# Performance work log

Hardware: AMD Instinct MI355X
Metric: run time of the kernel (lower is better)

Reference implementation:

```python
import jax, jax.numpy as jnp
import numpy as np
from jax import lax

B, T, S = 64, 512, 500
M, E, P, H, A = 80, 512, 256, 1024, 128
F_LOC, K_LOC = 32, 31
P_ATT_DROP, P_DEC_DROP, P_PRENET_DROP = 0.1, 0.1, 0.5
NEG_INF = -1e9


def _dropout(x, p, key):
    keep = jax.random.bernoulli(key, 1.0 - p, x.shape)
    return jnp.where(keep, x / (1.0 - p), jnp.zeros_like(x))


def _lstm_cell(x, h, c, w_ih, w_hh, b_ih, b_hh):
    # torch LSTMCell gate order: i, f, g, o
    gates = x @ w_ih.T + b_ih + h @ w_hh.T + b_hh
    i, f, g, o = jnp.split(gates, 4, axis=-1)
    c_new = jax.nn.sigmoid(f) * c + jax.nn.sigmoid(i) * jnp.tanh(g)
    h_new = jax.nn.sigmoid(o) * jnp.tanh(c_new)
    return h_new, c_new


def setup_inputs() -> dict:
    key = jax.random.key(0)
    ks = jax.random.split(key, 20)
    s = 0.02
    return dict(
        memory=jax.random.normal(ks[0], (B, T, E), jnp.float32),
        memory_lengths=jax.random.randint(ks[1], (B,), T // 2, T + 1),
        decoder_inputs=jax.random.normal(ks[2], (B, S, M), jnp.float32),
        prenet_w1=jax.random.normal(ks[3], (P, M), jnp.float32) * s,
        prenet_w2=jax.random.normal(ks[4], (P, P), jnp.float32) * s,
        attn_rnn_w_ih=jax.random.normal(ks[5], (4 * H, P + E), jnp.float32) * s,
        attn_rnn_w_hh=jax.random.normal(ks[6], (4 * H, H), jnp.float32) * s,
        attn_rnn_b_ih=jnp.zeros((4 * H,), jnp.float32),
        attn_rnn_b_hh=jnp.zeros((4 * H,), jnp.float32),
        dec_rnn_w_ih=jax.random.normal(ks[7], (4 * H, H + E), jnp.float32) * s,
        dec_rnn_w_hh=jax.random.normal(ks[8], (4 * H, H), jnp.float32) * s,
        dec_rnn_b_ih=jnp.zeros((4 * H,), jnp.float32),
        dec_rnn_b_hh=jnp.zeros((4 * H,), jnp.float32),
        attn_query_w=jax.random.normal(ks[9], (A, H), jnp.float32) * s,
        attn_memory_w=jax.random.normal(ks[10], (A, E), jnp.float32) * s,
        attn_v=jax.random.normal(ks[11], (A,), jnp.float32) * s,
        loc_conv_w=jax.random.normal(ks[12], (F_LOC, 2, K_LOC), jnp.float32) * s,
        loc_dense_w=jax.random.normal(ks[13], (A, F_LOC), jnp.float32) * s,
        proj_w=jax.random.normal(ks[14], (M, H + E), jnp.float32) * s,
        proj_b=jnp.zeros((M,), jnp.float32),
        gate_w=jax.random.normal(ks[15], (1, H + E), jnp.float32) * s,
        gate_b=jnp.zeros((1,), jnp.float32),
    )


def _forward(memory, memory_lengths, decoder_inputs,
             prenet_w1, prenet_w2,
             attn_rnn_w_ih, attn_rnn_w_hh, attn_rnn_b_ih, attn_rnn_b_hh,
             dec_rnn_w_ih, dec_rnn_w_hh, dec_rnn_b_ih, dec_rnn_b_hh,
             attn_query_w, attn_memory_w, attn_v, loc_conv_w, loc_dense_w,
             proj_w, proj_b, gate_w, gate_b):
    dt = memory.dtype
    # processed memory: [B, T, A]
    processed_memory = jnp.einsum('bte,ae->bta', memory, attn_memory_w)
    # mask True at padded positions
    pad_mask = jnp.arange(T)[None, :] >= memory_lengths[:, None]  # [B, T]

    # prenet over [S+1, B, M] (go frame + teacher-forced inputs); always-on dropout 0.5
    go = jnp.zeros((1, B, M), dt)
    x = jnp.concatenate([go, jnp.transpose(decoder_inputs, (1, 0, 2))], axis=0)
    x = _dropout(jax.nn.relu(x @ prenet_w1.T), P_PRENET_DROP, jax.random.key(101))
    x = _dropout(jax.nn.relu(x @ prenet_w2.T), P_PRENET_DROP, jax.random.key(102))
    prenet_out = x[:S]  # [S, B, P]

    drop_base = jax.random.key(7)
    pad = (K_LOC - 1) // 2

    def step(carry, xs):
        ah, ac, dh, dc, aw, awc, ctx = carry
        xt, t_idx = xs
        # attention RNN
        cell_in = jnp.concatenate([xt, ctx], axis=-1)  # [B, P+E]
        ah, ac = _lstm_cell(cell_in, ah, ac, attn_rnn_w_ih, attn_rnn_w_hh,
                            attn_rnn_b_ih, attn_rnn_b_hh)
        ah = _dropout(ah, P_ATT_DROP, jax.random.fold_in(drop_base, 2 * t_idx))
        # location-sensitive attention
        aw_cat = jnp.stack([aw, awc], axis=1)  # [B, 2, T]
        loc = lax.conv_general_dilated(aw_cat, loc_conv_w, (1,), [(pad, pad)],
                                       dimension_numbers=('NCH', 'OIH', 'NCH'))  # [B, F, T]
        processed_loc = jnp.einsum('bft,af->bta', loc, loc_dense_w)  # [B, T, A]
        q = (ah @ attn_query_w.T)[:, None, :]  # [B, 1, A]
        energies = jnp.tanh(q + processed_loc + processed_memory) @ attn_v  # [B, T]
        energies = jnp.where(pad_mask, NEG_INF, energies)
        aw = jax.nn.softmax(energies, axis=-1)
        ctx = jnp.einsum('bt,bte->be', aw, memory)
        awc = awc + aw
        # decoder RNN
        dec_in = jnp.concatenate([ah, ctx], axis=-1)  # [B, H+E]
        dh, dc = _lstm_cell(dec_in, dh, dc, dec_rnn_w_ih, dec_rnn_w_hh,
                            dec_rnn_b_ih, dec_rnn_b_hh)
        dh = _dropout(dh, P_DEC_DROP, jax.random.fold_in(drop_base, 2 * t_idx + 1))
        hc = jnp.concatenate([dh, ctx], axis=-1)  # [B, H+E]
        mel = hc @ proj_w.T + proj_b  # [B, M]
        gate = (hc @ gate_w.T + gate_b)[:, 0]  # [B]
        return (ah, ac, dh, dc, aw, awc, ctx), (mel, gate, aw)

    z = lambda *shape: jnp.zeros(shape, dt)
    carry0 = (z(B, H), z(B, H), z(B, H), z(B, H), z(B, T), z(B, T), z(B, E))
    _, (mels, gates, aligns) = lax.scan(step, carry0, (prenet_out, jnp.arange(S)))
    mel_outputs = jnp.transpose(mels, (1, 0, 2))      # [B, S, M]
    gate_outputs = jnp.transpose(gates, (1, 0))       # [B, S]
    alignments = jnp.transpose(aligns, (1, 0, 2))     # [B, S, T]
    return mel_outputs, gate_outputs, alignments


def reference(memory, memory_lengths, decoder_inputs,
              prenet_w1, prenet_w2,
              attn_rnn_w_ih, attn_rnn_w_hh, attn_rnn_b_ih, attn_rnn_b_hh,
              dec_rnn_w_ih, dec_rnn_w_hh, dec_rnn_b_ih, dec_rnn_b_hh,
              attn_query_w, attn_memory_w, attn_v, loc_conv_w, loc_dense_w,
              proj_w, proj_b, gate_w, gate_b):
    return _forward(memory, memory_lengths, decoder_inputs,
                    prenet_w1, prenet_w2,
                    attn_rnn_w_ih, attn_rnn_w_hh, attn_rnn_b_ih, attn_rnn_b_hh,
                    dec_rnn_w_ih, dec_rnn_w_hh, dec_rnn_b_ih, dec_rnn_b_hh,
                    attn_query_w, attn_memory_w, attn_v, loc_conv_w, loc_dense_w,
                    proj_w, proj_b, gate_w, gate_b)
```

## Files before the change

### kernel.cpp

```cpp
#include <hip/hip_runtime.h>
#include <cstdint>


__device__ __forceinline__ void tf2x32(uint32_t k0, uint32_t k1, uint32_t& x0, uint32_t& x1) {
  uint32_t ks2 = k0 ^ k1 ^ 0x1BD11BDAu;
  x0 += k0; x1 += k1;
#define TFR(r) { x0 += x1; x1 = (x1 << (r)) | (x1 >> (32 - (r))); x1 ^= x0; }
  TFR(13) TFR(15) TFR(26) TFR(6)
  x0 += k1; x1 += ks2 + 1u;
  TFR(17) TFR(29) TFR(16) TFR(24)
  x0 += ks2; x1 += k0 + 2u;
  TFR(13) TFR(15) TFR(26) TFR(6)
  x0 += k0; x1 += k1 + 3u;
  TFR(17) TFR(29) TFR(16) TFR(24)
  x0 += k1; x1 += ks2 + 4u;
  TFR(13) TFR(15) TFR(26) TFR(6)
  x0 += ks2; x1 += k0 + 5u;
#undef TFR
}

__device__ __forceinline__ uint32_t rng_bits(uint32_t k0, uint32_t k1, uint32_t idx) {
  uint32_t x0 = 0u, x1 = idx;
  tf2x32(k0, k1, x0, x1);
  return x0 ^ x1;
// ... 111 lines not shown
  const int jrow = jbase + row;

  float4 rx0, rx1, rw0, rw1;
  auto loadt = [&](int kb, float4& x0r, float4& x1r, float4& w0r, float4& w1r) {
    const float* xp; int xst, xof;
    if (kb < L0)            { xp = s0; xst = L0;   xof = kb; }
    else if (kb < L0 + L1)  { xp = s1; xst = L1;   xof = kb - L0; }
    else                    { xp = sh; xst = 1024; xof = kb - L0 - L1; }
    const float* xr = xp + (size_t)row * xst + xof + q8;
    x0r = *(const float4*)xr; x1r = *(const float4*)(xr + 4);
    const float* wp; int wst, wof;
    if (kb < LIH) { wp = wih; wst = LIH;  wof = kb; }
    else          { wp = whh; wst = 1024; wof = kb - LIH; }
    const float* wr = wp + (size_t)jrow * wst + wof + q8;
    w0r = *(const float4*)wr; w1r = *(const float4*)(wr + 4);
  };

  loadt(k0, rx0, rx1, rw0, rw1);
  float acc[4][4] = {};
  for (int c = 0; c < NC; ++c) {
    __syncthreads();
#pragma unroll
    for (int i = 0; i < 4; i++) {
      xs[q8 + i][row]     = ((const float*)&rx0)[i];
      xs[q8 + 4 + i][row] = ((const float*)&rx1)[i];
      ws[q8 + i][row]     = ((const float*)&rw0)[i];
      ws[q8 + 4 + i][row] = ((const float*)&rw1)[i];
    }
    __syncthreads();
    if (c + 1 < NC) loadt(k0 + (c + 1) * 32, rx0, rx1, rw0, rw1);
#pragma unroll
    for (int kk = 0; kk < 32; kk++) {
      float4 xv = *(const float4*)&xs[kk][bq * 4];
      float4 wv = *(const float4*)&ws[kk][jq * 4];
      acc[0][0] = fmaf(wv.x, xv.x, acc[0][0]); acc[0][1] = fmaf(wv.x, xv.y, acc[0][1]);
      acc[0][2] = fmaf(wv.x, xv.z, acc[0][2]); acc[0][3] = fmaf(wv.x, xv.w, acc[0][3]);
      acc[1][0] = fmaf(wv.y, xv.x, acc[1][0]); acc[1][1] = fmaf(wv.y, xv.y, acc[1][1]);
      acc[1][2] = fmaf(wv.y, xv.z, acc[1][2]); acc[1][3] = fmaf(wv.y, xv.w, acc[1][3]);
      acc[2][0] = fmaf(wv.z, xv.x, acc[2][0]); acc[2][1] = fmaf(wv.z, xv.y, acc[2][1]);
      acc[2][2] = fmaf(wv.z, xv.z, acc[2][2]); acc[2][3] = fmaf(wv.z, xv.w, acc[2][3]);
      acc[3][0] = fmaf(wv.w, xv.x, acc[3][0]); acc[3][1] = fmaf(wv.w, xv.y, acc[3][1]);
      acc[3][2] = fmaf(wv.w, xv.z, acc[3][2]); acc[3][3] = fmaf(wv.w, xv.w, acc[3][3]);
    }
  }
  float* pbase = part + (size_t)blockIdx.y * 64 * 4096;
#pragma unroll
  for (int bb = 0; bb < 4; bb++) {
    int b = bq * 4 + bb;
    float4 o = make_float4(acc[0][bb], acc[1][bb], acc[2][bb], acc[3][bb]);
    *(float4*)&pbase[(size_t)b * 4096 + jbase + jq * 4] = o;
  }
}

__global__ __launch_bounds__(1024) void k_attn_point(
    const float* __restrict__ part,
    const float* __restrict__ bih, const float* __restrict__ bhh,
    float* __restrict__ ac, float* __restrict__ ah,
    const uint32_t* __restrict__ kf, int dsel,
    const float* __restrict__ wq, float* __restrict__ q) {
  const int b = blockIdx.x, tid = threadIdx.x;
  __shared__ float ahs[1024];
  __shared__ float qred[128][9];
  const uint32_t fk0 = kf[2 * dsel], fk1 = kf[2 * dsel + 1];
  {
    const int h = tid;
    float gi = bih[h] + bhh[h];
    float gf = bih[h + 1024] + bhh[h + 1024];
    float gg = bih[h + 2048] + bhh[h + 2048];
    float go = bih[h + 3072] + bhh[h + 3072];
    for (int ks = 0; ks < 8; ks++) {
      const float* p = part + (size_t)(ks * 64 + b) * 4096;
      gi += p[h]; gf += p[h + 1024]; gg += p[h + 2048]; go += p[h + 3072];
    }
    float c = sigmf(gf) * ac[b * 1024 + h] + sigmf(gi) * tanhf(gg);
    float hn = sigmf(go) * tanhf(c);
    ac[b * 1024 + h] = c;
    float u = rng_u01(fk0, fk1, (uint32_t)(b * 1024 + h));
    hn = (u < 0.9f) ? hn / 0.9f : 0.0f;
    ah[b * 1024 + h] = hn;
    ahs[h] = hn;
  }
  __syncthreads();
  {
    const int a = tid & 127, seg = tid >> 7;
    const float* wr = wq + (size_t)a * 1024 + seg * 128;
    const float* hs = ahs + seg * 128;
    float a0 = 0, a1 = 0, a2 = 0, a3 = 0;
#pragma unroll 8
    for (int k = 0; k < 128; k += 4) {
      float4 w4 = *(const float4*)(wr + k);
      float4 h4 = *(const float4*)(hs + k);
      a0 = fmaf(h4.x, w4.x, a0); a1 = fmaf(h4.y, w4.y, a1);
      a2 = fmaf(h4.z, w4.z, a2); a3 = fmaf(h4.w, w4.w, a3);
    }
    qred[a][seg] = (a0 + a1) + (a2 + a3);
  }
  __syncthreads();
  if (tid < 128) {
    float t = 0.f;
#pragma unroll
    for (int i = 0; i < 8; i++) t += qred[tid][i];
    q[b * 128 + tid] = t;
  }
}

__global__ __launch_bounds__(256) void k_energy(
    const float* __restrict__ aw, const float* __restrict__ awc,
    const float* __restrict__ q, const float* __restrict__ pm,
    const float* __restrict__ wconv, const float* __restrict__ wld,
    const float* __restrict__ v, const int* __restrict__ mlen,
    float* __restrict__ energ) {
  const int b = blockIdx.x;
  const int t0 = blockIdx.y * 64;
  const int tid = threadIdx.x;
  const int t = tid & 63, aq = tid >> 6;
  __shared__ float sa[2][96];
  __shared__ float sq[128], sv[128];
  __shared__ float sw[1984];
  __shared__ float sld[128][32];
  __shared__ float sloc[64][33];
  __shared__ float spart[64][4];
  for (int i = tid; i < 94; i += 256) {
    int tt = t0 - 15 + i;
    bool ok = (tt >= 0 && tt < 512);
    sa[0][i] = ok ? aw[b * 512 + tt] : 0.0f;
    sa[1][i] = ok ? awc[b * 512 + tt] : 0.0f;
  }
  if (tid < 128) { sq[tid] = q[b * 128 + tid]; sv[tid] = v[tid]; }
  for (int i = tid; i < 1984; i += 256) sw[i] = wconv[i];
  for (int i = tid; i < 4096; i += 256) ((float*)sld)[i] = wld[i];
  __syncthreads();
  const int len = mlen[b];
  const int tt = t0 + t;
  const bool act = (tt < len);
  if (act) {
    for (int f = aq * 8; f < aq * 8 + 8; f++) {
      const float* w0 = sw + f * 62;
      const float* w1 = w0 + 31;
      float a = 0;
#pragma unroll
      for (int k = 0; k < 31; k++) a += sa[0][t + k] * w0[k] + sa[1][t + k] * w1[k];
      sloc[t][f] = a;
    }
  }
  __syncthreads();
  if (act) {
    const float* pmr = pm + (size_t)(b * 512 + tt) * 128;
    float acc = 0;
    for (int a = aq * 32; a < aq * 32 + 32; a++) {
      float pl = 0;
#pragma unroll
      for (int f = 0; f < 32; f++) pl += sloc[t][f] * sld[a][f];
      float x = sq[a] + pl + pmr[a];
      float ex = __expf(2.0f * x);
      acc += sv[a] * (1.0f - 2.0f / (ex + 1.0f));
    }
    spart[t][aq] = acc;
  }
  __syncthreads();
  if (tid < 64) {
    int g = t0 + tid;
    float e = (g < len) ? (spart[tid][0] + spart[tid][1]) + (spart[tid][2] + spart[tid][3]) : -1e9f;
    energ[b * 512 + g] = e;
  }
}

__global__ __launch_bounds__(1024) void k_softmax_ctx(
    const float* __restrict__ energ, const int* __restrict__ mlen,
    const float* __restrict__ memv,
    float* __restrict__ aw, float* __restrict__ awc, float* __restrict__ ctx,
    float* __restrict__ out_align, int s) {
  const int b = blockIdx.x, tid = threadIdx.x;
  __shared__ float se[512];
  __shared__ float red[8];
  __shared__ float4 cred4[8][128];
  const int len = mlen[b];
  float x = 0.f;
  if (tid < 512) {
    float e = energ[b * 512 + tid];
    float m = e;
#pragma unroll
    for (int off = 32; off; off >>= 1) m = fmaxf(m, __shfl_xor(m, off, 64));
    if ((tid & 63) == 0) red[tid >> 6] = m;
  }
  __syncthreads();
  float maxv = fmaxf(fmaxf(fmaxf(red[0], red[1]), fmaxf(red[2], red[3])),
                     fmaxf(fmaxf(red[4], red[5]), fmaxf(red[6], red[7])));
  if (tid < 512) {
    float e = energ[b * 512 + tid];
    x = (tid < len) ? __expf(e - maxv) : 0.0f;
    float sm = x;
#pragma unroll
    for (int off = 32; off; off >>= 1) sm += __shfl_xor(sm, off, 64);
    __syncthreads();
    if ((tid & 63) == 0) red[tid >> 6] = sm;
  } else {
    __syncthreads();
  }
  __syncthreads();
  const float tot = ((red[0] + red[1]) + (red[2] + red[3])) +
                    ((red[4] + red[5]) + (red[6] + red[7]));
  if (tid < 512) {
    float awv = x / tot;
    se[tid] = awv;
    aw[b * 512 + tid] = awv;
    awc[b * 512 + tid] += awv;
    out_align[(size_t)b * 256000 + (size_t)s * 512 + tid] = awv;
  }
  __syncthreads();
  {
    const int e4 = tid & 127, tq = tid >> 7;
    const float4* mb = (const float4*)(memv + (size_t)b * 262144) + e4;
    float4 c = make_float4(0.f, 0.f, 0.f, 0.f);
    for (int t2 = tq; t2 < len; t2 += 8) {
      float w = se[t2];
      float4 mv = mb[(size_t)t2 * 128];
      c.x = fmaf(w, mv.x, c.x); c.y = fmaf(w, mv.y, c.y);
      c.z = fmaf(w, mv.z, c.z); c.w = fmaf(w, mv.w, c.w);
    }
    cred4[tq][e4] = c;
  }
  __syncthreads();
  if (tid < 128) {
    float4 c = cred4[0][tid];
#pragma unroll
    for (int i = 1; i < 8; i++) {
      float4 d = cred4[i][tid];
      c.x += d.x; c.y += d.y; c.z += d.z; c.w += d.w;
    }
    *(float4*)&ctx[b * 512 + tid * 4] = c;
  }
}

__global__ __launch_bounds__(1024) void k_dec_out(
    const float* __restrict__ part,
    const float* __restrict__ bih, const float* __restrict__ bhh,
    float* __restrict__ dc, float* __restrict__ dh,
    const uint32_t* __restrict__ kf, int dsel,
    const float* __restrict__ ctx,
    const float* __restrict__ projw, const float* __restrict__ projb,
    const float* __restrict__ gatew, const float* __restrict__ gateb,
    float* __restrict__ out_mel, float* __restrict__ out_gate, int s) {
  const int b = blockIdx.x, tid = threadIdx.x;
  __shared__ float hcs[1536];
  __shared__ float ored[128][9];
  const uint32_t fk0 = kf[2 * dsel], fk1 = kf[2 * dsel + 1];
  {
    const int h = tid;
    float gi = bih[h] + bhh[h];
    float gf = bih[h + 1024] + bhh[h + 1024];
    float gg = bih[h + 2048] + bhh[h + 2048];
    float go = bih[h + 3072] + bhh[h + 3072];
    for (int ks = 0; ks < 8; ks++) {
      const float* p = part + (size_t)(ks * 64 + b) * 4096;
      gi += p[h]; gf += p[h + 1024]; gg += p[h + 2048]; go += p[h + 3072];
    }
    float c = sigmf(gf) * dc[b * 1024 + h] + sigmf(gi) * tanhf(gg);
    float hn = sigmf(go) * tanhf(c);
    dc[b * 1024 + h] = c;
    float u = rng_u01(fk0, fk1, (uint32_t)(b * 1024 + h));
    hn = (u < 0.9f) ? hn / 0.9f : 0.0f;
    dh[b * 1024 + h] = hn;
    hcs[h] = hn;
  }
  if (tid < 512) hcs[1024 + tid] = ctx[b * 512 + tid];
  __syncthreads();
  {
    const int mm = tid & 127, seg = tid >> 7;
    if (mm <= 80) {
      const float* wr = ((mm < 80) ? (projw + (size_t)mm * 1536) : gatew) + seg * 192;
      const float* hs = hcs + seg * 192;
      float a0 = 0, a1 = 0, a2 = 0, a3 = 0;
#pragma unroll 4
      for (int k = 0; k < 192; k += 4) {
        float4 w4 = *(const float4*)(wr + k);
        float4 h4 = *(const float4*)(hs + k);
        a0 = fmaf(h4.x, w4.x, a0); a1 = fmaf(h4.y, w4.y, a1);
        a2 = fmaf(h4.z, w4.z, a2); a3 = fmaf(h4.w, w4.w, a3);
      }
      ored[mm][seg] = (a0 + a1) + (a2 + a3);
    }
  }
  __syncthreads();
  if (tid <= 80) {
    float tot = 0.f;
#pragma unroll
    for (int i = 0; i < 8; i++) tot += ored[tid][i];
    if (tid < 80) out_mel[(size_t)b * 40000 + (size_t)s * 80 + tid] = tot + projb[tid];
    else          out_gate[b * 500 + s] = tot + gateb[0];
  }
}

extern "C" void kernel_launch(void* const* d_in, const int* in_sizes, int n_in,
                              void* d_out, int out_size, void* d_ws, size_t ws_size,
                              hipStream_t stream) {
  const float* memory = (const float*)d_in[0];
  const int*   mlen   = (const int*)d_in[1];
  const float* dec_in = (const float*)d_in[2];
  const float* pw1    = (const float*)d_in[3];
  const float* pw2    = (const float*)d_in[4];
  const float* awih   = (const float*)d_in[5];
  const float* awhh   = (const float*)d_in[6];
  const float* abih   = (const float*)d_in[7];
  const float* abhh   = (const float*)d_in[8];
  const float* dwih   = (const float*)d_in[9];
  const float* dwhh   = (const float*)d_in[10];
  const float* dbih   = (const float*)d_in[11];
  const float* dbhh   = (const float*)d_in[12];
  const float* wq     = (const float*)d_in[13];
  const float* wm     = (const float*)d_in[14];
  const float* av     = (const float*)d_in[15];
  const float* wconv  = (const float*)d_in[16];
  const float* wld    = (const float*)d_in[17];
  const float* projw  = (const float*)d_in[18];
  const float* projb  = (const float*)d_in[19];
  const float* gatew  = (const float*)d_in[20];
  const float* gateb  = (const float*)d_in[21];

  float* out       = (float*)d_out;
  float* out_mel   = out;
  float* out_gate  = out + 2560000;
  float* out_align = out + 2592000;

  float* ws     = (float*)d_ws;
  float* pm     = ws;
  float* prenet = pm + 4194304;
  float* part   = prenet + 8192000;
  float* st     = part + 2097152;
  float* ah  = st;
  float* ac  = ah + 65536;
  float* dh  = ac + 65536;
  float* dc  = dh + 65536;
  float* aw  = dc + 65536;
  float* awc = aw + 32768;
  float* ctx = awc + 32768;
  float* q     = ctx + 32768;
  float* energ = q + 8192;
  uint32_t* kf = (uint32_t*)(energ + 32768);

  hipMemsetAsync(st, 0, (size_t)(4 * 65536 + 3 * 32768) * sizeof(float), stream);
  k_fold<<<4, 256, 0, stream>>>(kf);
  k_pm<<<4096, 256, 0, stream>>>(memory, wm, pm);
  k_prenet1<<<4000, 256, 0, stream>>>(dec_in, pw1, prenet);
  k_prenet2<<<4000, 256, 0, stream>>>(prenet, pw2);

  for (int s = 0; s < 500; s++) {
    k_gemm_part<<<dim3(64, 8), 256, 0, stream>>>(prenet + (size_t)s * 16384, 256,
                                                 ctx, 512, ah, awih, awhh, 768, 224, part);
    k_attn_point<<<64, 1024, 0, stream>>>(part, abih, abhh, ac, ah, kf, 2 * s, wq, q);
    k_energy<<<dim3(64, 8), 256, 0, stream>>>(aw, awc, q, pm, wconv, wld, av, mlen, energ);
    k_softmax_ctx<<<64, 1024, 0, stream>>>(energ, mlen, memory, aw, awc, ctx, out_align, s);
    k_gemm_part<<<dim3(64, 8), 256, 0, stream>>>(ah, 1024, ctx, 512, dh,
                                                 dwih, dwhh, 1536, 320, part);
    k_dec_out<<<64, 1024, 0, stream>>>(part, dbih, dbhh, dc, dh, kf, 2 * s + 1, ctx,
                                       projw, projb, gatew, gateb, out_mel, out_gate, s);
  }
}
```

Baseline: 62.82 ms.

## Fuse per-step attention, energy, softmax and decoder-output kernels into one launch

```diff
diff --git a/kernel.cpp b/kernel.cpp
--- a/kernel.cpp
+++ b/kernel.cpp
@@ -187,224 +187,58 @@
   }
 }
 
-__global__ __launch_bounds__(1024) void k_attn_point(
-    const float* __restrict__ part,
-    const float* __restrict__ bih, const float* __restrict__ bhh,
-    float* __restrict__ ac, float* __restrict__ ah,
-    const uint32_t* __restrict__ kf, int dsel,
-    const float* __restrict__ wq, float* __restrict__ q) {
-  const int b = blockIdx.x, tid = threadIdx.x;
-  __shared__ float ahs[1024];
-  __shared__ float qred[128][9];
-  const uint32_t fk0 = kf[2 * dsel], fk1 = kf[2 * dsel + 1];
+
+struct FP {
+  const float* part_a; const float* part_d;
+  const float* abih; const float* abhh;
+  const float* dbih; const float* dbhh;
+  float* ac; float* ah; float* dc; float* dh;
+  const uint32_t* kf; int s;
+  const float* wq; const float* wconv; const float* wld; const float* av;
+  const float* pm; const int* mlen;
+  float* aw; float* awc;
+  const float* memory;
+  const float* ctx_prev; float* ctx_cur;
+  const float* projw; const float* projb;
+  const float* gatew; const float* gateb;
+  float* out_mel; float* out_gate; float* out_align;
+};
+
+union FU {
+  struct { float hcs[1536]; float ored[128][9]; } mg;
+  struct { float ahs[1024]; float qred[128][9]; } ap;
+  struct { float sa[2][160]; float sloc[128][33]; float spart[128][8]; } en;
+  struct { float cred[8][128][4]; } cx;
+};
+
+__device__ __forceinline__ void dec_pointwise_melgate(
+    const FP& p, FU& u, int b, int tid, int sm1) {
+  const uint32_t fk0 = p.kf[2 * (2 * sm1 + 1)], fk1 = p.kf[2 * (2 * sm1 + 1) + 1];
   {
     const int h = tid;
-    float gi = bih[h] + bhh[h];
-    float gf = bih[h + 1024] + bhh[h + 1024];
-    float gg = bih[h + 2048] + bhh[h + 2048];
-    float go = bih[h + 3072] + bhh[h + 3072];
+    float gi = p.dbih[h] + p.dbhh[h];
+    float gf = p.dbih[h + 1024] + p.dbhh[h + 1024];
+    float gg = p.dbih[h + 2048] + p.dbhh[h + 2048];
+    float go = p.dbih[h + 3072] + p.dbhh[h + 3072];
     for (int ks = 0; ks < 8; ks++) {
-      const float* p = part + (size_t)(ks * 64 + b) * 4096;
-      gi += p[h]; gf += p[h + 1024]; gg += p[h + 2048]; go += p[h + 3072];
-    }
-    float c = sigmf(gf) * ac[b * 1024 + h] + sigmf(gi) * tanhf(gg);
+      const float* pp = p.part_d + (size_t)(ks * 64 + b) * 4096;
+      gi += pp[h]; gf += pp[h + 1024]; gg += pp[h + 2048]; go += pp[h + 3072];
+    }
+    float c = sigmf(gf) * p.dc[b * 1024 + h] + sigmf(gi) * tanhf(gg);
     float hn = sigmf(go) * tanhf(c);
-    ac[b * 1024 + h] = c;
-    float u = rng_u01(fk0, fk1, (uint32_t)(b * 1024 + h));
-    hn = (u < 0.9f) ? hn / 0.9f : 0.0f;
-    ah[b * 1024 + h] = hn;
-    ahs[h] = hn;
-  }
-  __syncthreads();
-  {
-    const int a = tid & 127, seg = tid >> 7;
-    const float* wr = wq + (size_t)a * 1024 + seg * 128;
-    const float* hs = ahs + seg * 128;
-    float a0 = 0, a1 = 0, a2 = 0, a3 = 0;
-#pragma unroll 8
-    for (int k = 0; k < 128; k += 4) {
-      float4 w4 = *(const float4*)(wr + k);
-      float4 h4 = *(const float4*)(hs + k);
-      a0 = fmaf(h4.x, w4.x, a0); a1 = fmaf(h4.y, w4.y, a1);
-      a2 = fmaf(h4.z, w4.z, a2); a3 = fmaf(h4.w, w4.w, a3);
-    }
-    qred[a][seg] = (a0 + a1) + (a2 + a3);
-  }
-  __syncthreads();
-  if (tid < 128) {
-    float t = 0.f;
-#pragma unroll
-    for (int i = 0; i < 8; i++) t += qred[tid][i];
-    q[b * 128 + tid] = t;
-  }
-}
-
-__global__ __launch_bounds__(256) void k_energy(
-    const float* __restrict__ aw, const float* __restrict__ awc,
-    const float* __restrict__ q, const float* __restrict__ pm,
-    const float* __restrict__ wconv, const float* __restrict__ wld,
-    const float* __restrict__ v, const int* __restrict__ mlen,
-    float* __restrict__ energ) {
-  const int b = blockIdx.x;
-  const int t0 = blockIdx.y * 64;
-  const int tid = threadIdx.x;
-  const int t = tid & 63, aq = tid >> 6;
-  __shared__ float sa[2][96];
-  __shared__ float sq[128], sv[128];
-  __shared__ float sw[1984];
-  __shared__ float sld[128][32];
-  __shared__ float sloc[64][33];
-  __shared__ float spart[64][4];
-  for (int i = tid; i < 94; i += 256) {
-    int tt = t0 - 15 + i;
-    bool ok = (tt >= 0 && tt < 512);
-    sa[0][i] = ok ? aw[b * 512 + tt] : 0.0f;
-    sa[1][i] = ok ? awc[b * 512 + tt] : 0.0f;
-  }
-  if (tid < 128) { sq[tid] = q[b * 128 + tid]; sv[tid] = v[tid]; }
-  for (int i = tid; i < 1984; i += 256) sw[i] = wconv[i];
-  for (int i = tid; i < 4096; i += 256) ((float*)sld)[i] = wld[i];
-  __syncthreads();
-  const int len = mlen[b];
-  const int tt = t0 + t;
-  const bool act = (tt < len);
-  if (act) {
-    for (int f = aq * 8; f < aq * 8 + 8; f++) {
-      const float* w0 = sw + f * 62;
-      const float* w1 = w0 + 31;
-      float a = 0;
-#pragma unroll
-      for (int k = 0; k < 31; k++) a += sa[0][t + k] * w0[k] + sa[1][t + k] * w1[k];
-      sloc[t][f] = a;
-    }
-  }
-  __syncthreads();
-  if (act) {
-    const float* pmr = pm + (size_t)(b * 512 + tt) * 128;
-    float acc = 0;
-    for (int a = aq * 32; a < aq * 32 + 32; a++) {
-      float pl = 0;
-#pragma unroll
-      for (int f = 0; f < 32; f++) pl += sloc[t][f] * sld[a][f];
-      float x = sq[a] + pl + pmr[a];
-      float ex = __expf(2.0f * x);
-      acc += sv[a] * (1.0f - 2.0f / (ex + 1.0f));
-    }
-    spart[t][aq] = acc;
-  }
-  __syncthreads();
-  if (tid < 64) {
-    int g = t0 + tid;
-    float e = (g < len) ? (spart[tid][0] + spart[tid][1]) + (spart[tid][2] + spart[tid][3]) : -1e9f;
-    energ[b * 512 + g] = e;
-  }
-}
-
-__global__ __launch_bounds__(1024) void k_softmax_ctx(
-    const float* __restrict__ energ, const int* __restrict__ mlen,
-    const float* __restrict__ memv,
-    float* __restrict__ aw, float* __restrict__ awc, float* __restrict__ ctx,
-    float* __restrict__ out_align, int s) {
-  const int b = blockIdx.x, tid = threadIdx.x;
-  __shared__ float se[512];
-  __shared__ float red[8];
-  __shared__ float4 cred4[8][128];
-  const int len = mlen[b];
-  float x = 0.f;
-  if (tid < 512) {
-    float e = energ[b * 512 + tid];
-    float m = e;
-#pragma unroll
-    for (int off = 32; off; off >>= 1) m = fmaxf(m, __shfl_xor(m, off, 64));
-    if ((tid & 63) == 0) red[tid >> 6] = m;
-  }
-  __syncthreads();
-  float maxv = fmaxf(fmaxf(fmaxf(red[0], red[1]), fmaxf(red[2], red[3])),
-                     fmaxf(fmaxf(red[4], red[5]), fmaxf(red[6], red[7])));
-  if (tid < 512) {
-    float e = energ[b * 512 + tid];
-    x = (tid < len) ? __expf(e - maxv) : 0.0f;
-    float sm = x;
-#pragma unroll
-    for (int off = 32; off; off >>= 1) sm += __shfl_xor(sm, off, 64);
-    __syncthreads();
-    if ((tid & 63) == 0) red[tid >> 6] = sm;
-  } else {
-    __syncthreads();
-  }
-  __syncthreads();
-  const float tot = ((red[0] + red[1]) + (red[2] + red[3])) +
-                    ((red[4] + red[5]) + (red[6] + red[7]));
-  if (tid < 512) {
-    float awv = x / tot;
-    se[tid] = awv;
-    aw[b * 512 + tid] = awv;
-    awc[b * 512 + tid] += awv;
-    out_align[(size_t)b * 256000 + (size_t)s * 512 + tid] = awv;
-  }
-  __syncthreads();
-  {
-    const int e4 = tid & 127, tq = tid >> 7;
-    const float4* mb = (const float4*)(memv + (size_t)b * 262144) + e4;
-    float4 c = make_float4(0.f, 0.f, 0.f, 0.f);
-    for (int t2 = tq; t2 < len; t2 += 8) {
-      float w = se[t2];
-      float4 mv = mb[(size_t)t2 * 128];
-      c.x = fmaf(w, mv.x, c.x); c.y = fmaf(w, mv.y, c.y);
-      c.z = fmaf(w, mv.z, c.z); c.w = fmaf(w, mv.w, c.w);
-    }
-    cred4[tq][e4] = c;
-  }
-  __syncthreads();
-  if (tid < 128) {
-    float4 c = cred4[0][tid];
-#pragma unroll
-    for (int i = 1; i < 8; i++) {
-      float4 d = cred4[i][tid];
-      c.x += d.x; c.y += d.y; c.z += d.z; c.w += d.w;
-    }
-    *(float4*)&ctx[b * 512 + tid * 4] = c;
-  }
-}
-
-__global__ __launch_bounds__(1024) void k_dec_out(
-    const float* __restrict__ part,
-    const float* __restrict__ bih, const float* __restrict__ bhh,
-    float* __restrict__ dc, float* __restrict__ dh,
-    const uint32_t* __restrict__ kf, int dsel,
-    const float* __restrict__ ctx,
-    const float* __restrict__ projw, const float* __restrict__ projb,
-    const float* __restrict__ gatew, const float* __restrict__ gateb,
-    float* __restrict__ out_mel, float* __restrict__ out_gate, int s) {
-  const int b = blockIdx.x, tid = threadIdx.x;
-  __shared__ float hcs[1536];
-  __shared__ float ored[128][9];
-  const uint32_t fk0 = kf[2 * dsel], fk1 = kf[2 * dsel + 1];
-  {
-    const int h = tid;
-    float gi = bih[h] + bhh[h];
-    float gf = bih[h + 1024] + bhh[h + 1024];
-    float gg = bih[h + 2048] + bhh[h + 2048];
-    float go = bih[h + 3072] + bhh[h + 3072];
-    for (int ks = 0; ks < 8; ks++) {
-      const float* p = part + (size_t)(ks * 64 + b) * 4096;
-      gi += p[h]; gf += p[h + 1024]; gg += p[h + 2048]; go += p[h + 3072];
-    }
-    float c = sigmf(gf) * dc[b * 1024 + h] + sigmf(gi) * tanhf(gg);
-    float hn = sigmf(go) * tanhf(c);
-    dc[b * 1024 + h] = c;
-    float u = rng_u01(fk0, fk1, (uint32_t)(b * 1024 + h));
-    hn = (u < 0.9f) ? hn / 0.9f : 0.0f;
-    dh[b * 1024 + h] = hn;
-    hcs[h] = hn;
-  }
-  if (tid < 512) hcs[1024 + tid] = ctx[b * 512 + tid];
+    p.dc[b * 1024 + h] = c;
+    float uu = rng_u01(fk0, fk1, (uint32_t)(b * 1024 + h));
+    hn = (uu < 0.9f) ? hn / 0.9f : 0.0f;
+    p.dh[b * 1024 + h] = hn;
+    u.mg.hcs[h] = hn;
+  }
+  if (tid < 512) u.mg.hcs[1024 + tid] = p.ctx_prev[b * 512 + tid];
   __syncthreads();
   {
     const int mm = tid & 127, seg = tid >> 7;
     if (mm <= 80) {
-      const float* wr = ((mm < 80) ? (projw + (size_t)mm * 1536) : gatew) + seg * 192;
-      const float* hs = hcs + seg * 192;
+      const float* wr = ((mm < 80) ? (p.projw + (size_t)mm * 1536) : p.gatew) + seg * 192;
+      const float* hs = u.mg.hcs + seg * 192;
       float a0 = 0, a1 = 0, a2 = 0, a3 = 0;
 #pragma unroll 4
       for (int k = 0; k < 192; k += 4) {
@@ -413,17 +247,196 @@
         a0 = fmaf(h4.x, w4.x, a0); a1 = fmaf(h4.y, w4.y, a1);
         a2 = fmaf(h4.z, w4.z, a2); a3 = fmaf(h4.w, w4.w, a3);
       }
-      ored[mm][seg] = (a0 + a1) + (a2 + a3);
+      u.mg.ored[mm][seg] = (a0 + a1) + (a2 + a3);
     }
   }
   __syncthreads();
   if (tid <= 80) {
     float tot = 0.f;
 #pragma unroll
-    for (int i = 0; i < 8; i++) tot += ored[tid][i];
-    if (tid < 80) out_mel[(size_t)b * 40000 + (size_t)s * 80 + tid] = tot + projb[tid];
-    else          out_gate[b * 500 + s] = tot + gateb[0];
-  }
+    for (int i = 0; i < 8; i++) tot += u.mg.ored[tid][i];
+    if (tid < 80) p.out_mel[(size_t)b * 40000 + (size_t)sm1 * 80 + tid] = tot + p.projb[tid];
+    else          p.out_gate[b * 500 + sm1] = tot + p.gateb[0];
+  }
+  __syncthreads();
+}
+
+__global__ __launch_bounds__(1024) void k_fused(FP p) {
+  const int b = blockIdx.x, tid = threadIdx.x;
+  __shared__ FU u;
+  __shared__ float q_s[128], sv[128], se[512], red[8];
+  __shared__ float sw[1984];
+  __shared__ float sld[128][32];
+
+  if (p.s > 0) dec_pointwise_melgate(p, u, b, tid, p.s - 1);
+
+  {
+    const uint32_t fk0 = p.kf[4 * p.s], fk1 = p.kf[4 * p.s + 1];
+    const int h = tid;
+    float gi = p.abih[h] + p.abhh[h];
+    float gf = p.abih[h + 1024] + p.abhh[h + 1024];
+    float gg = p.abih[h + 2048] + p.abhh[h + 2048];
+    float go = p.abih[h + 3072] + p.abhh[h + 3072];
+    for (int ks = 0; ks < 8; ks++) {
+      const float* pp = p.part_a + (size_t)(ks * 64 + b) * 4096;
+      gi += pp[h]; gf += pp[h + 1024]; gg += pp[h + 2048]; go += pp[h + 3072];
+    }
+    float c = sigmf(gf) * p.ac[b * 1024 + h] + sigmf(gi) * tanhf(gg);
+    float hn = sigmf(go) * tanhf(c);
+    p.ac[b * 1024 + h] = c;
+    float uu = rng_u01(fk0, fk1, (uint32_t)(b * 1024 + h));
+    hn = (uu < 0.9f) ? hn / 0.9f : 0.0f;
+    p.ah[b * 1024 + h] = hn;
+    u.ap.ahs[h] = hn;
+  }
+  __syncthreads();
+  {
+    const int a = tid & 127, seg = tid >> 7;
+    const float* wr = p.wq + (size_t)a * 1024 + seg * 128;
+    const float* hs = u.ap.ahs + seg * 128;
+    float a0 = 0, a1 = 0, a2 = 0, a3 = 0;
+#pragma unroll 8
+    for (int k = 0; k < 128; k += 4) {
+      float4 w4 = *(const float4*)(wr + k);
+      float4 h4 = *(const float4*)(hs + k);
+      a0 = fmaf(h4.x, w4.x, a0); a1 = fmaf(h4.y, w4.y, a1);
+      a2 = fmaf(h4.z, w4.z, a2); a3 = fmaf(h4.w, w4.w, a3);
+    }
+    u.ap.qred[a][seg] = (a0 + a1) + (a2 + a3);
+  }
+  __syncthreads();
+  if (tid < 128) {
+    float t = 0.f;
+#pragma unroll
+    for (int i = 0; i < 8; i++) t += u.ap.qred[tid][i];
+    q_s[tid] = t;
+  }
+  for (int i = tid; i < 1984; i += 1024) sw[i] = p.wconv[i];
+  for (int i = tid; i < 4096; i += 1024) ((float*)sld)[i] = p.wld[i];
+  if (tid >= 128 && tid < 256) sv[tid - 128] = p.av[tid - 128];
+
+  const int len = p.mlen[b];
+  for (int tile = 0; tile < 4; tile++) {
+    const int t0 = tile * 128;
+    __syncthreads();
+    for (int i = tid; i < 158; i += 1024) {
+      int tt = t0 - 15 + i;
+      bool ok = (tt >= 0 && tt < 512);
+      u.en.sa[0][i] = ok ? p.aw[b * 512 + tt] : 0.f;
+      u.en.sa[1][i] = ok ? p.awc[b * 512 + tt] : 0.f;
+    }
+    __syncthreads();
+    {
+      const int t = tid & 127, fq = tid >> 7;
+#pragma unroll
+      for (int df = 0; df < 4; df++) {
+        int f = fq * 4 + df;
+        const float* w0 = sw + f * 62;
+        const float* w1 = w0 + 31;
+        float a = 0.f;
+#pragma unroll
+        for (int k = 0; k < 31; k++)
+          a = fmaf(u.en.sa[0][t + k], w0[k], fmaf(u.en.sa[1][t + k], w1[k], a));
+        u.en.sloc[t][f] = a;
+      }
+    }
+    __syncthreads();
+    {
+      const int t = tid & 127, aq = tid >> 7;
+      const int tt = t0 + t;
+      float acc = 0.f;
+      if (tt < len) {
+        const float* pmr = p.pm + (size_t)(b * 512 + tt) * 128;
+        const float* slr = u.en.sloc[t];
+        for (int j = 0; j < 16; j++) {
+          int a = aq * 16 + j;
+          const float* wl = sld[a];
+          float pl = 0.f;
+#pragma unroll
+          for (int f4 = 0; f4 < 8; f4++) {
+            float4 w4 = *(const float4*)(wl + f4 * 4);
+            pl = fmaf(slr[f4 * 4], w4.x, pl); pl = fmaf(slr[f4 * 4 + 1], w4.y, pl);
+            pl = fmaf(slr[f4 * 4 + 2], w4.z, pl); pl = fmaf(slr[f4 * 4 + 3], w4.w, pl);
+          }
+          float x = q_s[a] + pl + pmr[a];
+          float ex = __expf(2.0f * x);
+          acc = fmaf(sv[a], 1.0f - 2.0f / (ex + 1.0f), acc);
+        }
+      }
+      u.en.spart[t][aq] = acc;
+    }
+    __syncthreads();
+    if (tid < 128) {
+      int tt = t0 + tid;
+      float e = 0.f;
+#pragma unroll
+      for (int i = 0; i < 8; i++) e += u.en.spart[tid][i];
+      se[tt] = (tt < len) ? e : -1e9f;
+    }
+  }
+  __syncthreads();
+
+  float x = 0.f;
+  if (tid < 512) {
+    float e = se[tid];
+    float m = e;
+#pragma unroll
+    for (int off = 32; off; off >>= 1) m = fmaxf(m, __shfl_xor(m, off, 64));
+    if ((tid & 63) == 0) red[tid >> 6] = m;
+  }
+  __syncthreads();
+  const float maxv = fmaxf(fmaxf(fmaxf(red[0], red[1]), fmaxf(red[2], red[3])),
+                           fmaxf(fmaxf(red[4], red[5]), fmaxf(red[6], red[7])));
+  if (tid < 512) {
+    x = (tid < len) ? __expf(se[tid] - maxv) : 0.0f;
+    float sm = x;
+#pragma unroll
+    for (int off = 32; off; off >>= 1) sm += __shfl_xor(sm, off, 64);
+    __syncthreads();
+    if ((tid & 63) == 0) red[tid >> 6] = sm;
+  } else {
+    __syncthreads();
+  }
+  __syncthreads();
+  const float tot = ((red[0] + red[1]) + (red[2] + red[3])) +
+                    ((red[4] + red[5]) + (red[6] + red[7]));
+  if (tid < 512) {
+    float awv = x / tot;
+    se[tid] = awv;
+    p.aw[b * 512 + tid] = awv;
+    p.awc[b * 512 + tid] += awv;
+    p.out_align[(size_t)b * 256000 + (size_t)p.s * 512 + tid] = awv;
+  }
+  __syncthreads();
+
+  {
+    const int e4 = tid & 127, tq = tid >> 7;
+    const float4* mb = (const float4*)(p.memory + (size_t)b * 262144) + e4;
+    float4 c = make_float4(0.f, 0.f, 0.f, 0.f);
+    for (int t2 = tq; t2 < len; t2 += 8) {
+      float w = se[t2];
+      float4 mv = mb[(size_t)t2 * 128];
+      c.x = fmaf(w, mv.x, c.x); c.y = fmaf(w, mv.y, c.y);
+      c.z = fmaf(w, mv.z, c.z); c.w = fmaf(w, mv.w, c.w);
+    }
+    *(float4*)&u.cx.cred[tq][e4][0] = c;
+  }
+  __syncthreads();
+  if (tid < 128) {
+    float4 c = *(float4*)&u.cx.cred[0][tid][0];
+#pragma unroll
+    for (int i = 1; i < 8; i++) {
+      float4 d = *(float4*)&u.cx.cred[i][tid][0];
+      c.x += d.x; c.y += d.y; c.z += d.z; c.w += d.w;
+    }
+    *(float4*)&p.ctx_cur[b * 512 + tid * 4] = c;
+  }
+}
+
+__global__ __launch_bounds__(1024) void k_dec_final(FP p) {
+  const int b = blockIdx.x, tid = threadIdx.x;
+  __shared__ FU u;
+  dec_pointwise_melgate(p, u, b, tid, 499);
 }
 
 extern "C" void kernel_launch(void* const* d_in, const int* in_sizes, int n_in,
@@ -457,37 +470,51 @@
   float* out_gate  = out + 2560000;
   float* out_align = out + 2592000;
 
-  float* ws     = (float*)d_ws;
-  float* pm     = ws;
-  float* prenet = pm + 4194304;
-  float* part   = prenet + 8192000;
-  float* st     = part + 2097152;
-  float* ah  = st;
-  float* ac  = ah + 65536;
-  float* dh  = ac + 65536;
-  float* dc  = dh + 65536;
-  float* aw  = dc + 65536;
-  float* awc = aw + 32768;
-  float* ctx = awc + 32768;
-  float* q     = ctx + 32768;
-  float* energ = q + 8192;
-  uint32_t* kf = (uint32_t*)(energ + 32768);
-
-  hipMemsetAsync(st, 0, (size_t)(4 * 65536 + 3 * 32768) * sizeof(float), stream);
+  float* ws      = (float*)d_ws;
+  float* pm      = ws;
+  float* prenet  = pm + 4194304;
+  float* part_a  = prenet + 8192000;
+  float* part_d  = part_a + 2097152;
+  float* st      = part_d + 2097152;
+  float* ah   = st;
+  float* ac   = ah + 65536;
+  float* dh   = ac + 65536;
+  float* dc   = dh + 65536;
+  float* aw   = dc + 65536;
+  float* awc  = aw + 32768;
+  float* ctx0 = awc + 32768;
+  float* ctx1 = ctx0 + 32768;
+  uint32_t* kf = (uint32_t*)(ctx1 + 32768);
+
+  hipMemsetAsync(st, 0, (size_t)(4 * 65536 + 4 * 32768) * sizeof(float), stream);
   k_fold<<<4, 256, 0, stream>>>(kf);
   k_pm<<<4096, 256, 0, stream>>>(memory, wm, pm);
   k_prenet1<<<4000, 256, 0, stream>>>(dec_in, pw1, prenet);
   k_prenet2<<<4000, 256, 0, stream>>>(prenet, pw2);
 
+  FP fp;
+  fp.part_a = part_a; fp.part_d = part_d;
+  fp.abih = abih; fp.abhh = abhh; fp.dbih = dbih; fp.dbhh = dbhh;
+  fp.ac = ac; fp.ah = ah; fp.dc = dc; fp.dh = dh;
+  fp.kf = kf;
+  fp.wq = wq; fp.wconv = wconv; fp.wld = wld; fp.av = av;
+  fp.pm = pm; fp.mlen = mlen;
+  fp.aw = aw; fp.awc = awc;
+  fp.memory = memory;
+  fp.projw = projw; fp.projb = projb; fp.gatew = gatew; fp.gateb = gateb;
+  fp.out_mel = out_mel; fp.out_gate = out_gate; fp.out_align = out_align;
+
+  float* ctxb[2] = { ctx0, ctx1 };
   for (int s = 0; s < 500; s++) {
+    float* ctx_prev = ctxb[(s + 1) & 1];
+    float* ctx_cur  = ctxb[s & 1];
     k_gemm_part<<<dim3(64, 8), 256, 0, stream>>>(prenet + (size_t)s * 16384, 256,
-                                                 ctx, 512, ah, awih, awhh, 768, 224, part);
-    k_attn_point<<<64, 1024, 0, stream>>>(part, abih, abhh, ac, ah, kf, 2 * s, wq, q);
-    k_energy<<<dim3(64, 8), 256, 0, stream>>>(aw, awc, q, pm, wconv, wld, av, mlen, energ);
-    k_softmax_ctx<<<64, 1024, 0, stream>>>(energ, mlen, memory, aw, awc, ctx, out_align, s);
-    k_gemm_part<<<dim3(64, 8), 256, 0, stream>>>(ah, 1024, ctx, 512, dh,
-                                                 dwih, dwhh, 1536, 320, part);
-    k_dec_out<<<64, 1024, 0, stream>>>(part, dbih, dbhh, dc, dh, kf, 2 * s + 1, ctx,
-                                       projw, projb, gatew, gateb, out_mel, out_gate, s);
-  }
-}
+                                                 ctx_prev, 512, ah, awih, awhh, 768, 224, part_a);
+    fp.s = s; fp.ctx_prev = ctx_prev; fp.ctx_cur = ctx_cur;
+    k_fused<<<64, 1024, 0, stream>>>(fp);
+    k_gemm_part<<<dim3(64, 8), 256, 0, stream>>>(ah, 1024, ctx_cur, 512, dh,
+                                                 dwih, dwhh, 1536, 320, part_d);
+  }
+  fp.ctx_prev = ctxb[1];
+  k_dec_final<<<64, 1024, 0, stream>>>(fp);
+}
```

New measurement: 84.58 ms. 34.6% more time.

## Split pointwise LSTM/softmax kernels across hidden quarters and defer mel projection one step

Applied to the files above, without the earlier changes.

```diff
diff --git a/kernel.cpp b/kernel.cpp
--- a/kernel.cpp
+++ b/kernel.cpp
@@ -187,18 +187,19 @@
   }
 }
 
-__global__ __launch_bounds__(1024) void k_attn_point(
+__global__ __launch_bounds__(256) void k_attn_pw(
     const float* __restrict__ part,
     const float* __restrict__ bih, const float* __restrict__ bhh,
     float* __restrict__ ac, float* __restrict__ ah,
-    const uint32_t* __restrict__ kf, int dsel,
-    const float* __restrict__ wq, float* __restrict__ q) {
-  const int b = blockIdx.x, tid = threadIdx.x;
-  __shared__ float ahs[1024];
-  __shared__ float qred[128][9];
-  const uint32_t fk0 = kf[2 * dsel], fk1 = kf[2 * dsel + 1];
+    const uint32_t* __restrict__ kf, int s,
+    const float* __restrict__ wq, float* __restrict__ qp) {
+  const int b = blockIdx.x, hq = blockIdx.y, tid = threadIdx.x;
+  __shared__ float ahs[256];
+  __shared__ float wtile[128][65];
+  __shared__ float qred[128][2];
+  const uint32_t fk0 = kf[4 * s], fk1 = kf[4 * s + 1];
   {
-    const int h = tid;
+    const int h = hq * 256 + tid;
     float gi = bih[h] + bhh[h];
     float gf = bih[h + 1024] + bhh[h + 1024];
     float gg = bih[h + 2048] + bhh[h + 2048];
@@ -213,35 +214,34 @@
     float u = rng_u01(fk0, fk1, (uint32_t)(b * 1024 + h));
     hn = (u < 0.9f) ? hn / 0.9f : 0.0f;
     ah[b * 1024 + h] = hn;
-    ahs[h] = hn;
-  }
-  __syncthreads();
-  {
-    const int a = tid & 127, seg = tid >> 7;
-    const float* wr = wq + (size_t)a * 1024 + seg * 128;
-    const float* hs = ahs + seg * 128;
-    float a0 = 0, a1 = 0, a2 = 0, a3 = 0;
-#pragma unroll 8
-    for (int k = 0; k < 128; k += 4) {
-      float4 w4 = *(const float4*)(wr + k);
-      float4 h4 = *(const float4*)(hs + k);
-      a0 = fmaf(h4.x, w4.x, a0); a1 = fmaf(h4.y, w4.y, a1);
-      a2 = fmaf(h4.z, w4.z, a2); a3 = fmaf(h4.w, w4.w, a3);
-    }
-    qred[a][seg] = (a0 + a1) + (a2 + a3);
-  }
-  __syncthreads();
-  if (tid < 128) {
-    float t = 0.f;
-#pragma unroll
-    for (int i = 0; i < 8; i++) t += qred[tid][i];
-    q[b * 128 + tid] = t;
-  }
+    ahs[tid] = hn;
+  }
+  const int a = tid & 127, kh = tid >> 7;
+  float acc = 0.f;
+  for (int sub = 0; sub < 4; sub++) {
+    const int kbase = hq * 256 + sub * 64;
+    __syncthreads();
+#pragma unroll
+    for (int j = 0; j < 8; j++) {
+      int idx = tid + j * 256;
+      int row = idx >> 4, kc = (idx & 15) << 2;
+      *(float4*)&wtile[row][kc] = *(const float4*)&wq[(size_t)row * 1024 + kbase + kc];
+    }
+    __syncthreads();
+    const float* wr = &wtile[a][kh * 32];
+    const float* hr = &ahs[sub * 64 + kh * 32];
+#pragma unroll
+    for (int kk = 0; kk < 32; kk++) acc = fmaf(hr[kk], wr[kk], acc);
+  }
+  qred[a][kh] = acc;
+  __syncthreads();
+  if (tid < 128)
+    qp[(size_t)(hq * 64 + b) * 128 + tid] = qred[tid][0] + qred[tid][1];
 }
 
 __global__ __launch_bounds__(256) void k_energy(
     const float* __restrict__ aw, const float* __restrict__ awc,
-    const float* __restrict__ q, const float* __restrict__ pm,
+    const float* __restrict__ qp, const float* __restrict__ pm,
     const float* __restrict__ wconv, const float* __restrict__ wld,
     const float* __restrict__ v, const int* __restrict__ mlen,
     float* __restrict__ energ) {
@@ -261,7 +261,11 @@
     sa[0][i] = ok ? aw[b * 512 + tt] : 0.0f;
     sa[1][i] = ok ? awc[b * 512 + tt] : 0.0f;
   }
-  if (tid < 128) { sq[tid] = q[b * 128 + tid]; sv[tid] = v[tid]; }
+  if (tid < 128) {
+    sq[tid] = qp[(size_t)b * 128 + tid] + qp[(size_t)(64 + b) * 128 + tid] +
+              qp[(size_t)(128 + b) * 128 + tid] + qp[(size_t)(192 + b) * 128 + tid];
+    sv[tid] = v[tid];
+  }
   for (int i = tid; i < 1984; i += 256) sw[i] = wconv[i];
   for (int i = tid; i < 4096; i += 256) ((float*)sld)[i] = wld[i];
   __syncthreads();
@@ -300,52 +304,45 @@
   }
 }
 
-__global__ __launch_bounds__(1024) void k_softmax_ctx(
+__global__ __launch_bounds__(256) void k_softmax_ctx(
     const float* __restrict__ energ, const int* __restrict__ mlen,
     const float* __restrict__ memv,
     float* __restrict__ aw, float* __restrict__ awc, float* __restrict__ ctx,
     float* __restrict__ out_align, int s) {
-  const int b = blockIdx.x, tid = threadIdx.x;
+  const int b = blockIdx.x, ec = blockIdx.y, tid = threadIdx.x;
   __shared__ float se[512];
-  __shared__ float red[8];
-  __shared__ float4 cred4[8][128];
+  __shared__ float red[4];
+  __shared__ float cred[8][132];
   const int len = mlen[b];
-  float x = 0.f;
-  if (tid < 512) {
-    float e = energ[b * 512 + tid];
-    float m = e;
-#pragma unroll
-    for (int off = 32; off; off >>= 1) m = fmaxf(m, __shfl_xor(m, off, 64));
-    if ((tid & 63) == 0) red[tid >> 6] = m;
-  }
-  __syncthreads();
-  float maxv = fmaxf(fmaxf(fmaxf(red[0], red[1]), fmaxf(red[2], red[3])),
-                     fmaxf(fmaxf(red[4], red[5]), fmaxf(red[6], red[7])));
-  if (tid < 512) {
-    float e = energ[b * 512 + tid];
-    x = (tid < len) ? __expf(e - maxv) : 0.0f;
-    float sm = x;
-#pragma unroll
-    for (int off = 32; off; off >>= 1) sm += __shfl_xor(sm, off, 64);
-    __syncthreads();
-    if ((tid & 63) == 0) red[tid >> 6] = sm;
-  } else {
-    __syncthreads();
-  }
-  __syncthreads();
-  const float tot = ((red[0] + red[1]) + (red[2] + red[3])) +
-                    ((red[4] + red[5]) + (red[6] + red[7]));
-  if (tid < 512) {
-    float awv = x / tot;
-    se[tid] = awv;
-    aw[b * 512 + tid] = awv;
-    awc[b * 512 + tid] += awv;
-    out_align[(size_t)b * 256000 + (size_t)s * 512 + tid] = awv;
+  const float e0 = energ[b * 512 + tid];
+  const float e1 = energ[b * 512 + 256 + tid];
+  float m = fmaxf(e0, e1);
+#pragma unroll
+  for (int off = 32; off; off >>= 1) m = fmaxf(m, __shfl_xor(m, off, 64));
+  if ((tid & 63) == 0) red[tid >> 6] = m;
+  __syncthreads();
+  const float maxv = fmaxf(fmaxf(red[0], red[1]), fmaxf(red[2], red[3]));
+  const float x0 = __expf(e0 - maxv);
+  const float x1 = (tid + 256 < len) ? __expf(e1 - maxv) : 0.0f;
+  float sm = x0 + x1;
+#pragma unroll
+  for (int off = 32; off; off >>= 1) sm += __shfl_xor(sm, off, 64);
+  __syncthreads();
+  if ((tid & 63) == 0) red[tid >> 6] = sm;
+  __syncthreads();
+  const float tot = (red[0] + red[1]) + (red[2] + red[3]);
+  const float a0 = x0 / tot, a1 = x1 / tot;
+  se[tid] = a0; se[tid + 256] = a1;
+  if (ec == 0) {
+    aw[b * 512 + tid] = a0; aw[b * 512 + 256 + tid] = a1;
+    awc[b * 512 + tid] += a0; awc[b * 512 + 256 + tid] += a1;
+    float* oa = out_align + (size_t)b * 256000 + (size_t)s * 512;
+    oa[tid] = a0; oa[tid + 256] = a1;
   }
   __syncthreads();
   {
-    const int e4 = tid & 127, tq = tid >> 7;
-    const float4* mb = (const float4*)(memv + (size_t)b * 262144) + e4;
+    const int c4 = tid & 31, tq = tid >> 5;
+    const float4* mb = (const float4*)(memv + (size_t)b * 262144 + ec * 128) + c4;
     float4 c = make_float4(0.f, 0.f, 0.f, 0.f);
     for (int t2 = tq; t2 < len; t2 += 8) {
       float w = se[t2];
@@ -353,35 +350,66 @@
       c.x = fmaf(w, mv.x, c.x); c.y = fmaf(w, mv.y, c.y);
       c.z = fmaf(w, mv.z, c.z); c.w = fmaf(w, mv.w, c.w);
     }
-    cred4[tq][e4] = c;
-  }
-  __syncthreads();
-  if (tid < 128) {
-    float4 c = cred4[0][tid];
+    *(float4*)&cred[tq][c4 * 4] = c;
+  }
+  __syncthreads();
+  if (tid < 32) {
+    float4 c = *(float4*)&cred[0][tid * 4];
 #pragma unroll
     for (int i = 1; i < 8; i++) {
-      float4 d = cred4[i][tid];
+      float4 d = *(float4*)&cred[i][tid * 4];
       c.x += d.x; c.y += d.y; c.z += d.z; c.w += d.w;
     }
-    *(float4*)&ctx[b * 512 + tid * 4] = c;
-  }
-}
-
-__global__ __launch_bounds__(1024) void k_dec_out(
+    *(float4*)&ctx[b * 512 + ec * 128 + tid * 4] = c;
+  }
+}
+
+__device__ __forceinline__ void melgate_body(
+    int b, int sIdx, const float* __restrict__ dhp, const float* __restrict__ ctxp,
+    const float* __restrict__ projw, const float* __restrict__ projb,
+    const float* __restrict__ gatew, const float* __restrict__ gateb,
+    float* __restrict__ out_mel, float* __restrict__ out_gate, int tid,
+    float* __restrict__ hcs , float (*ored)[2] ) {
+  for (int i = tid; i < 1536; i += 256)
+    hcs[i] = (i < 1024) ? dhp[b * 1024 + i] : ctxp[b * 512 + (i - 1024)];
+  __syncthreads();
+  const int mm = tid & 127, seg = tid >> 7;
+  if (mm <= 80) {
+    const float* wr = ((mm < 80) ? (projw + (size_t)mm * 1536) : gatew) + seg * 768;
+    const float* hs = hcs + seg * 768;
+    float a0 = 0, a1 = 0, a2 = 0, a3 = 0;
+#pragma unroll 4
+    for (int k = 0; k < 768; k += 4) {
+      float4 w4 = *(const float4*)(wr + k);
+      float4 h4 = *(const float4*)(hs + k);
+      a0 = fmaf(h4.x, w4.x, a0); a1 = fmaf(h4.y, w4.y, a1);
+      a2 = fmaf(h4.z, w4.z, a2); a3 = fmaf(h4.w, w4.w, a3);
+    }
+    ored[mm][seg] = (a0 + a1) + (a2 + a3);
+  }
+  __syncthreads();
+  if (tid <= 80) {
+    float tot = ored[tid][0] + ored[tid][1];
+    if (tid < 80) out_mel[(size_t)b * 40000 + (size_t)sIdx * 80 + tid] = tot + projb[tid];
+    else          out_gate[b * 500 + sIdx] = tot + gateb[0];
+  }
+}
+
+__global__ __launch_bounds__(256) void k_dec_pw(
     const float* __restrict__ part,
     const float* __restrict__ bih, const float* __restrict__ bhh,
-    float* __restrict__ dc, float* __restrict__ dh,
-    const uint32_t* __restrict__ kf, int dsel,
-    const float* __restrict__ ctx,
+    float* __restrict__ dc, float* __restrict__ dhn,
+    const uint32_t* __restrict__ kf, int s,
+    const float* __restrict__ dhp, const float* __restrict__ ctxp,
     const float* __restrict__ projw, const float* __restrict__ projb,
     const float* __restrict__ gatew, const float* __restrict__ gateb,
-    float* __restrict__ out_mel, float* __restrict__ out_gate, int s) {
-  const int b = blockIdx.x, tid = threadIdx.x;
+    float* __restrict__ out_mel, float* __restrict__ out_gate) {
+  const int b = blockIdx.x, hq = blockIdx.y, tid = threadIdx.x;
   __shared__ float hcs[1536];
-  __shared__ float ored[128][9];
-  const uint32_t fk0 = kf[2 * dsel], fk1 = kf[2 * dsel + 1];
+  __shared__ float ored[128][2];
+  const uint32_t fk0 = kf[4 * s + 2], fk1 = kf[4 * s + 3];
   {
-    const int h = tid;
+    const int h = hq * 256 + tid;
     float gi = bih[h] + bhh[h];
     float gf = bih[h + 1024] + bhh[h + 1024];
     float gg = bih[h + 2048] + bhh[h + 2048];
@@ -395,35 +423,23 @@
     dc[b * 1024 + h] = c;
     float u = rng_u01(fk0, fk1, (uint32_t)(b * 1024 + h));
     hn = (u < 0.9f) ? hn / 0.9f : 0.0f;
-    dh[b * 1024 + h] = hn;
-    hcs[h] = hn;
-  }
-  if (tid < 512) hcs[1024 + tid] = ctx[b * 512 + tid];
-  __syncthreads();
-  {
-    const int mm = tid & 127, seg = tid >> 7;
-    if (mm <= 80) {
-      const float* wr = ((mm < 80) ? (projw + (size_t)mm * 1536) : gatew) + seg * 192;
-      const float* hs = hcs + seg * 192;
-      float a0 = 0, a1 = 0, a2 = 0, a3 = 0;
-#pragma unroll 4
-      for (int k = 0; k < 192; k += 4) {
-        float4 w4 = *(const float4*)(wr + k);
-        float4 h4 = *(const float4*)(hs + k);
-        a0 = fmaf(h4.x, w4.x, a0); a1 = fmaf(h4.y, w4.y, a1);
-        a2 = fmaf(h4.z, w4.z, a2); a3 = fmaf(h4.w, w4.w, a3);
-      }
-      ored[mm][seg] = (a0 + a1) + (a2 + a3);
-    }
-  }
-  __syncthreads();
-  if (tid <= 80) {
-    float tot = 0.f;
-#pragma unroll
-    for (int i = 0; i < 8; i++) tot += ored[tid][i];
-    if (tid < 80) out_mel[(size_t)b * 40000 + (size_t)s * 80 + tid] = tot + projb[tid];
-    else          out_gate[b * 500 + s] = tot + gateb[0];
-  }
+    dhn[b * 1024 + h] = hn;
+  }
+  if (hq == 0 && s > 0) {
+    melgate_body(b, s - 1, dhp, ctxp, projw, projb, gatew, gateb,
+                 out_mel, out_gate, tid, hcs, ored);
+  }
+}
+
+__global__ __launch_bounds__(256) void k_mel_final(
+    const float* __restrict__ dhp, const float* __restrict__ ctxp,
+    const float* __restrict__ projw, const float* __restrict__ projb,
+    const float* __restrict__ gatew, const float* __restrict__ gateb,
+    float* __restrict__ out_mel, float* __restrict__ out_gate) {
+  __shared__ float hcs[1536];
+  __shared__ float ored[128][2];
+  melgate_body(blockIdx.x, 499, dhp, ctxp, projw, projb, gatew, gateb,
+               out_mel, out_gate, threadIdx.x, hcs, ored);
 }
 
 extern "C" void kernel_launch(void* const* d_in, const int* in_sizes, int n_in,
@@ -457,37 +473,50 @@
   float* out_gate  = out + 2560000;
   float* out_align = out + 2592000;
 
-  float* ws     = (float*)d_ws;
-  float* pm     = ws;
-  float* prenet = pm + 4194304;
-  float* part   = prenet + 8192000;
-  float* st     = part + 2097152;
-  float* ah  = st;
-  float* ac  = ah + 65536;
-  float* dh  = ac + 65536;
-  float* dc  = dh + 65536;
-  float* aw  = dc + 65536;
-  float* awc = aw + 32768;
-  float* ctx = awc + 32768;
-  float* q     = ctx + 32768;
-  float* energ = q + 8192;
+  float* ws      = (float*)d_ws;
+  float* pm      = ws;
+  float* prenet  = pm + 4194304;
+  float* part_a  = prenet + 8192000;
+  float* part_d  = part_a + 2097152;
+  float* st      = part_d + 2097152;
+  float* ah   = st;
+  float* ac   = ah + 65536;
+  float* dh0  = ac + 65536;
+  float* dh1  = dh0 + 65536;
+  float* dc   = dh1 + 65536;
+  float* aw   = dc + 65536;
+  float* awc  = aw + 32768;
+  float* ctx0 = awc + 32768;
+  float* ctx1 = ctx0 + 32768;
+  float* qp   = ctx1 + 32768;
+  float* energ = qp + 32768;
   uint32_t* kf = (uint32_t*)(energ + 32768);
 
-  hipMemsetAsync(st, 0, (size_t)(4 * 65536 + 3 * 32768) * sizeof(float), stream);
+  hipMemsetAsync(st, 0, (size_t)(5 * 65536 + 4 * 32768) * sizeof(float), stream);
   k_fold<<<4, 256, 0, stream>>>(kf);
   k_pm<<<4096, 256, 0, stream>>>(memory, wm, pm);
   k_prenet1<<<4000, 256, 0, stream>>>(dec_in, pw1, prenet);
   k_prenet2<<<4000, 256, 0, stream>>>(prenet, pw2);
 
+  float* dhb[2]  = { dh0, dh1 };
+  float* ctxb[2] = { ctx0, ctx1 };
   for (int s = 0; s < 500; s++) {
+    float* ctx_prev = ctxb[(s + 1) & 1];
+    float* ctx_cur  = ctxb[s & 1];
+    float* dh_prev  = dhb[s & 1];
+    float* dh_next  = dhb[(s + 1) & 1];
     k_gemm_part<<<dim3(64, 8), 256, 0, stream>>>(prenet + (size_t)s * 16384, 256,
-                                                 ctx, 512, ah, awih, awhh, 768, 224, part);
-    k_attn_point<<<64, 1024, 0, stream>>>(part, abih, abhh, ac, ah, kf, 2 * s, wq, q);
-    k_energy<<<dim3(64, 8), 256, 0, stream>>>(aw, awc, q, pm, wconv, wld, av, mlen, energ);
-    k_softmax_ctx<<<64, 1024, 0, stream>>>(energ, mlen, memory, aw, awc, ctx, out_align, s);
-    k_gemm_part<<<dim3(64, 8), 256, 0, stream>>>(ah, 1024, ctx, 512, dh,
-                                                 dwih, dwhh, 1536, 320, part);
-    k_dec_out<<<64, 1024, 0, stream>>>(part, dbih, dbhh, dc, dh, kf, 2 * s + 1, ctx,
-                                       projw, projb, gatew, gateb, out_mel, out_gate, s);
-  }
-}
+                                                 ctx_prev, 512, ah, awih, awhh, 768, 224, part_a);
+    k_attn_pw<<<dim3(64, 4), 256, 0, stream>>>(part_a, abih, abhh, ac, ah, kf, s, wq, qp);
+    k_energy<<<dim3(64, 8), 256, 0, stream>>>(aw, awc, qp, pm, wconv, wld, av, mlen, energ);
+    k_softmax_ctx<<<dim3(64, 4), 256, 0, stream>>>(energ, mlen, memory, aw, awc, ctx_cur,
+                                                   out_align, s);
+    k_gemm_part<<<dim3(64, 8), 256, 0, stream>>>(ah, 1024, ctx_cur, 512, dh_prev,
+                                                 dwih, dwhh, 1536, 320, part_d);
+    k_dec_pw<<<dim3(64, 4), 256, 0, stream>>>(part_d, dbih, dbhh, dc, dh_next, kf, s,
+                                              dh_prev, ctx_prev, projw, projb, gatew, gateb,
+                                              out_mel, out_gate);
+  }
+  k_mel_final<<<64, 256, 0, stream>>>(dh0, ctx1, projw, projb, gatew, gateb,
+                                      out_mel, out_gate);
+}
```

Measured after the change: 62.61 ms. No clear change (-0.3%).
